# Kernel optimization log

Hardware: AMD Instinct MI355X
Metric: run time of the kernel (lower is better)

## Reference

```python
import jax, jax.numpy as jnp
import numpy as np
from jax import lax

LAGS = np.array([1, 2, 3, 4, 5, 6, 7, 14, 21, 28])
MAX_LAG = int(LAGS.max())
N_LAGS = len(LAGS)
HID = 512
EMB_ROWS, EMB_DIM = 12, 5
BATCH, CTX, HOR = 128, 720, 168
T0 = CTX + HOR + MAX_LAG  # 916
IN_DIM = 1 + N_LAGS + 1 + EMB_DIM  # target + lags + log-scale + seq-cat embedding = 17


def _lstm_cell(x, h, c, Wih, Whh, bih, bhh):
    g = x @ Wih.T + h @ Whh.T + bih + bhh
    i, f, gg, o = jnp.split(g, 4, axis=-1)  # torch gate order i,f,g,o
    c = jax.nn.sigmoid(f) * c + jax.nn.sigmoid(i) * jnp.tanh(gg)
    h = jax.nn.sigmoid(o) * jnp.tanh(c)
    return h, c


def _run_layer(xs, params):
    Bn = xs.shape[0]
    z = jnp.zeros((Bn, HID), xs.dtype)
    def step(hc, x):
        h, c = _lstm_cell(x, hc[0], hc[1], *params)
        return (h, c), h
    hc, ys = lax.scan(step, (z, z), jnp.swapaxes(xs, 0, 1))
    return jnp.swapaxes(ys, 0, 1), hc


def _forward(X, pad_mask, emb, W_ih0, W_hh0, b_ih0, b_hh0,
             W_ih1, W_hh1, b_ih1, b_hh1, W_head, b_head, H, C):
    Bn = X.shape[0]
    p0 = (W_ih0, W_hh0, b_ih0, b_hh0)
    p1 = (W_ih1, W_hh1, b_ih1, b_hh1)
    X = X.at[:, -H:, 0].set(0.0)
    past = X[:, :X.shape[1] - H, 0][:, ::-1]  # [B, C+MAX_LAG], newest first
    Xt = X[:, MAX_LAG:]                       # [B, T, 2], T = C + H
    mask = pad_mask[:, MAX_LAG:][:, :C].astype(X.dtype)
    scale = (jnp.abs(Xt[:, :C, 0]) * mask).sum(1) / jnp.clip(mask.sum(1), 1.0)
    scale = jnp.maximum(scale, 1e-10)         # [B]
    tgt = Xt[:, :, 0] / scale[:, None]        # scaled target
    past = past / scale[:, None]
    # context lag features: value at context step t is past[C-1-t]; lag l -> past[C-1-t+l]
    idx = (C - 1 - np.arange(C))[:, None] + LAGS[None, :]  # [C, N_LAGS], static
    lags_ctx = past[:, idx]                                # [B, C, N_LAGS]
    logscale = jnp.log(scale)[:, None]                     # [B, 1]
    seq_emb = emb[Xt[:, :, 1].astype(jnp.int32)]           # [B, T, EMB_DIM]
    x_ctx = jnp.concatenate([
        tgt[:, :C, None], lags_ctx,
        jnp.broadcast_to(logscale[:, None, :], (Bn, C, 1)),
        seq_emb[:, :C]], 2)                                # [B, C, IN_DIM]
    o1, hc1 = _run_layer(x_ctx, p0)
    o2, hc2 = _run_layer(o1, p1)
    y_ctx = o2 @ W_head.T + b_head                         # [B, C, 1]
    # per-step static decode features (log-scale + seq-cat embedding)
    feat_dec = jnp.concatenate([
        jnp.broadcast_to(logscale[:, None, :], (Bn, H - 1, 1)),
        seq_emb[:, C:C + H - 1]], 2)                       # [B, H-1, 1+EMB_DIM]
    lag_idx = LAGS - 1
    def dec_step(carry, feat):
        h1, c1, h2, c2, buf, prev = carry
        lag_t = buf[:, lag_idx]                            # [B, N_LAGS]
        # step input is clone().detach()'d in the original -> stop_gradient
        x_t = lax.stop_gradient(jnp.concatenate([prev[:, None], lag_t, feat], 1))
        h1, c1 = _lstm_cell(x_t, h1, c1, *p0)
        h2, c2 = _lstm_cell(h1, h2, c2, *p1)
        o = h2 @ W_head.T + b_head                         # [B, 1]
        buf = jnp.concatenate([prev[:, None], buf[:, :-1]], 1)
        return (h1, c1, h2, c2, buf, o[:, 0]), o
    carry0 = (hc1[0], hc1[1], hc2[0], hc2[1], past[:, :MAX_LAG], y_ctx[:, -1, 0])
    _, y_dec = lax.scan(dec_step, carry0, jnp.swapaxes(feat_dec, 0, 1))
    y_hat = jnp.concatenate([y_ctx, jnp.swapaxes(y_dec, 0, 1)], 1)  # [B, C+H-1, 1]
    return y_hat * scale[:, None, None]


def setup_inputs():
    key = jax.random.key(0)
    ks = jax.random.split(key, 10)
    s = 0.05
    tgt = jax.random.normal(ks[0], (BATCH, T0, 1), jnp.float32)
    cat = jax.random.randint(ks[1], (BATCH, T0, 1), 0, EMB_ROWS).astype(jnp.float32)
    return {
        "X": jnp.concatenate([tgt, cat], 2),
        "pad_mask": jnp.ones((BATCH, T0), dtype=bool),
        "emb": jax.random.normal(ks[2], (EMB_ROWS, EMB_DIM), jnp.float32) * s,
        "W_ih0": jax.random.normal(ks[3], (4 * HID, IN_DIM), jnp.float32) * s,
        "W_hh0": jax.random.normal(ks[4], (4 * HID, HID), jnp.float32) * s,
        "b_ih0": jnp.zeros((4 * HID,), jnp.float32),
        "b_hh0": jnp.zeros((4 * HID,), jnp.float32),
        "W_ih1": jax.random.normal(ks[5], (4 * HID, HID), jnp.float32) * s,
        "W_hh1": jax.random.normal(ks[6], (4 * HID, HID), jnp.float32) * s,
        "b_ih1": jnp.zeros((4 * HID,), jnp.float32),
        "b_hh1": jnp.zeros((4 * HID,), jnp.float32),
        "W_head": jax.random.normal(ks[7], (1, HID), jnp.float32) * s,
        "b_head": jnp.zeros((1,), jnp.float32),
        "H": HOR,
        "context_length": CTX,
    }


def reference(X, pad_mask, emb, W_ih0, W_hh0, b_ih0, b_hh0,
              W_ih1, W_hh1, b_ih1, b_hh1, W_head, b_head, H, context_length):
    return _forward(X, pad_mask, emb, W_ih0, W_hh0, b_ih0, b_hh0,
                    W_ih1, W_hh1, b_ih1, b_hh1, W_head, b_head, H, context_length)
```

## Files before the change

kernel.cpp:

```cpp
#include <hip/hip_runtime.h>
#include <math.h>


#define CTXL   720
#define MAXLAG 28
#define TT0    916
#define NSTEP  887
#define OUTW   887
#define HS2    (128 * 256)

typedef _Float16 h2v   __attribute__((ext_vector_type(2)));
typedef _Float16 half8 __attribute__((ext_vector_type(8)));
typedef float    f32x4 __attribute__((ext_vector_type(4)));

struct Prm {
  const float* __restrict__ Wih0; const float* __restrict__ Whh0;
  const float* __restrict__ bih0; const float* __restrict__ bhh0;
  const float* __restrict__ Wih1; const float* __restrict__ Whh1;
  const float* __restrict__ bih1; const float* __restrict__ bhh1;
  const float* __restrict__ Whead; const float* __restrict__ bhead;
  const float* __restrict__ scale; const float* __restrict__ ls;
  const float* __restrict__ V; const float* __restrict__ embf;
  unsigned* __restrict__ H0; unsigned* __restrict__ H1;
  float* __restrict__ Ypart;
  float* __restrict__ out;
  int* __restrict__ bar;
};

__device__ __forceinline__ void stb(float* p, float v) {
  __hip_atomic_store(p, v, __ATOMIC_RELAXED, __HIP_MEMORY_SCOPE_AGENT);
}
__device__ __forceinline__ void stbu(unsigned* p, unsigned v) {
  __hip_atomic_store(p, v, __ATOMIC_RELAXED, __HIP_MEMORY_SCOPE_AGENT);
}
__device__ __forceinline__ float ldb(const float* p) {
  return __hip_atomic_load(p, __ATOMIC_RELAXED, __HIP_MEMORY_SCOPE_AGENT);
}
__device__ __forceinline__ int ldbi(const int* p) {
  return __hip_atomic_load(p, __ATOMIC_RELAXED, __HIP_MEMORY_SCOPE_AGENT);
}
__device__ __forceinline__ uint2 ldbu2(const unsigned* p) {
  union { unsigned long long u; uint2 v; } cv;
  cv.u = __hip_atomic_load((const unsigned long long*)p, __ATOMIC_RELAXED,
                           __HIP_MEMORY_SCOPE_AGENT);
  return cv.v;
}
__device__ __forceinline__ float sigm(float x) {
  return __builtin_amdgcn_rcpf(1.f + __expf(-x));
}
__device__ __forceinline__ float tanh_f(float x) {
  return fmaf(2.f, __builtin_amdgcn_rcpf(1.f + __expf(-2.f * x)), -1.f);
}
__device__ __forceinline__ unsigned packh2(float a, float b) {
  union { h2v h; unsigned u; } cv;
  cv.h = h2v{(_Float16)a, (_Float16)b};
  return cv.u;
}

__global__ void prep_kernel(const float* __restrict__ X, const float* __restrict__ emb,
                            float* __restrict__ scale, float* __restrict__ ls,
                            float* __restrict__ V, float* __restrict__ embf,
                            unsigned* __restrict__ zb , int* __restrict__ bar)
{
    const int bid = blockIdx.x, tid = threadIdx.x;
    if (bid < 128) {
        const int b = bid;
        __shared__ float sred[256];
        __shared__ float s_scale;
        float p = 0.f;
        for (int t = tid; t < CTXL; t += 256)
            p += fabsf(X[(size_t)(b * TT0 + MAXLAG + t) * 2]);
        sred[tid] = p; __syncthreads();
        for (int s = 128; s > 0; s >>= 1) {
            if (tid < s) sred[tid] += sred[tid + s];
            __syncthreads();
        }
        if (tid == 0) {
            float sc = fmaxf(sred[0] / (float)CTXL, 1e-10f);
            s_scale = sc; scale[b] = sc; ls[b] = logf(sc);
        }
        __syncthreads();
        const float sc = s_scale;
        for (int j = tid; j < TT0 - 168; j += 256)
            V[(size_t)j * 128 + b] = X[(size_t)(b * TT0 + j) * 2] / sc;
        for (int t = tid; t < NSTEP; t += 256) {
            int cc = (int)X[(size_t)(b * TT0 + MAXLAG + t) * 2 + 1];
            #pragma unroll
            for (int d = 0; d < 5; ++d)
                embf[((size_t)t * 5 + d) * 128 + b] = emb[cc * 5 + d];
        }
    } else {
        const int ZT = 4 * HS2;
        for (int idx = (bid - 128) * 256 + tid; idx < ZT; idx += 128 * 256)
            zb[idx] = 0u;
        if (bid == 128) { bar[tid] = 0; bar[256 + tid] = 0; }
    }
}

#define STAGE(LDSBUF, GSRC) { _Pragma("unroll")                               \
    for (int r_ = 0; r_ < 2; ++r_) {                                          \
      const int ch_ = tid + r_ * 512;                                         \
      const int sl_ = ch_ >> 6, c_ = ch_ & 63;                                \
      const unsigned* gp_ = (GSRC) + (size_t)(S0 + sl_) * 256 + c_ * 4;       \
      const uint2 a_ = ldbu2(gp_), b_ = ldbu2(gp_ + 2);                       \
      *(uint4*)&(LDSBUF)[sl_ * 256 + ((c_ * 4) ^ ((sl_ & 7) << 2))] =         \
          make_uint4(a_.x, a_.y, b_.x, b_.y); } }

#define MMPASS_L1(D) { _Pragma("unroll")                                      \
    for (int t_ = 0; t_ < 16; ++t_) {                                         \
      union { uint4 u; half8 h; } b0_, b1_;                                   \
      b0_.u = *(const uint4*)&h0lds[ar * 256 + ((t_ * 16 + akg * 4) ^ xsw)];  \
      b1_.u = *(const uint4*)&h1lds[ar * 256 + ((t_ * 16 + akg * 4) ^ xsw)];  \
      D = __builtin_amdgcn_mfma_f32_16x16x32_f16(awA[t_], b0_.h, D, 0, 0, 0); \
      D = __builtin_amdgcn_mfma_f32_16x16x32_f16(awB[t_], b1_.h, D, 0, 0, 0); } }

#define MMPASS_L0(D) { _Pragma("unroll")                                      \
    for (int t_ = 0; t_ < 16; ++t_) {                                         \
      union { uint4 u; half8 h; } b0_;                                        \
      b0_.u = *(const uint4*)&h0lds[ar * 256 + ((t_ * 16 + akg * 4) ^ xsw)];  \
      D = __builtin_amdgcn_mfma_f32_16x16x32_f16(awA[t_], b0_.h, D, 0, 0, 0); } }

#define XDOT(G, XF) { const int ub_ = (T * 4 + akg) * 68;                     \
    _Pragma("unroll")                                                         \
    for (int q_ = 0; q_ < 4; ++q_) { float xd_ = b4[q_];                      \
      _Pragma("unroll")                                                       \
      for (int j_ = 0; j_ < 17; ++j_)                                         \
          xd_ = fmaf(sX0[ub_ + q_ * 17 + j_], (XF)[j_], xd_);                 \
      (G)[q_] += xd_; } }

#define OUTWRITE(PAR, STEP) {                                                 \
    float v_ = ldb(&p.Ypart[(size_t)(PAR) * 4096 + (S0 + (tid >> 5)) * 32 + (tid & 31)]); \
    v_ += __shfl_xor(v_, 1, 64); v_ += __shfl_xor(v_, 2, 64);                 \
    v_ += __shfl_xor(v_, 4, 64); v_ += __shfl_xor(v_, 8, 64);                 \
    v_ += __shfl_xor(v_, 16, 64);                                             \
    if ((l & 31) == 0)                                                        \
        stb(&p.out[(size_t)(S0 + (tid >> 5)) * OUTW + (STEP)],                \
            (v_ + bh_all) * sc_my); }

__global__ __launch_bounds__(512, 1) void deepar_persist(Prm p)
{
    const int tid = threadIdx.x, blk = blockIdx.x;
    const int ublk = blk >> 3, grp = blk & 7;
    const int U0 = ublk * 16, S0 = grp * 16;
    const int l = tid & 63, wv = tid >> 6;
    const int ar = l & 15, akg = l >> 4;
    const bool isL0 = (wv < 4);
    const int T = isL0 ? wv : (wv - 4);
    const int u = U0 + T * 4 + akg;
    const int sg = S0 + ar;
    const int xsw = (ar & 7) << 2;

    __shared__ unsigned h0lds[16 * 256];
    __shared__ unsigned h1lds[16 * 256];
    __shared__ float sX0[16 * 68];
    __shared__ float sYring[168 * 16];
    __shared__ float sYp[4][16];

    half8 awA[16], awB[16];
    {
        const int grow = ((ar & 3) << 9) + U0 + T * 4 + (ar >> 2);
        const float* srcA = isL0 ? p.Whh0 : p.Wih1;
        #pragma unroll
        for (int t = 0; t < 16; ++t) {
            #pragma unroll
            for (int j = 0; j < 8; ++j) {
                const int k = t * 32 + akg * 8 + j;
                awA[t][j] = (_Float16)srcA[(size_t)grow * 512 + k];
            }
        }
        if (!isL0) {
            #pragma unroll
            for (int t = 0; t < 16; ++t) {
                #pragma unroll
                for (int j = 0; j < 8; ++j) {
                    const int k = t * 32 + akg * 8 + j;
                    awB[t][j] = (_Float16)p.Whh1[(size_t)grow * 512 + k];
                }
            }
        }
    }
    for (int idx = tid; idx < 1088; idx += 512) {
        const int ul = idx / 68, r = idx % 68;
        const int q = r / 17, j = r % 17;
        sX0[idx] = p.Wih0[((q << 9) + U0 + ul) * 17 + j];
    }

    float cc = 0.f;
    float b4[4];
    float lsv = 0.f, whm = 0.f;
    if (isL0) {
        #pragma unroll
        for (int q = 0; q < 4; ++q)
            b4[q] = p.bih0[(q << 9) + u] + p.bhh0[(q << 9) + u];
        lsv = p.ls[sg];
    } else {
        #pragma unroll
        for (int q = 0; q < 4; ++q)
            b4[q] = p.bih1[(q << 9) + u] + p.bhh1[(q << 9) + u];
        whm = p.Whead[u];
    }
    const float bh_all = p.bhead[0];
    const float sc_my = p.scale[S0 + (tid >> 5)];
    __syncthreads();

    f32x4 g0c = {0.f, 0.f, 0.f, 0.f};
    int ph = 0;
    const int LG[10] = {1, 2, 3, 4, 5, 6, 7, 14, 21, 28};
    int* gctr = p.bar + grp * 64;

    auto gbar_arrive = [&]() {
        asm volatile("s_waitcnt vmcnt(0)" ::: "memory");
        __syncthreads();
        ++ph;
        if (wv == 7 && l == 0)
            __hip_atomic_fetch_add(&gctr[(ublk & 3) * 16], 1,
                                   __ATOMIC_RELAXED, __HIP_MEMORY_SCOPE_AGENT);
    };
    auto gbar_wait = [&]() {
        if (wv == 7) {
            const int target = 32 * ph;
            for (;;) {
                int v = (l < 4) ? ldbi(&gctr[l * 16]) : 0;
                v += __shfl_xor(v, 1, 64); v += __shfl_xor(v, 2, 64);
                if (__shfl(v, 0, 64) >= target) break;
                __builtin_amdgcn_s_sleep(1);
            }
        }
        __syncthreads();
    };

    for (int P = 0; P <= CTXL; ++P) {
        STAGE(h0lds, p.H0 + (size_t)((P - 1) & 1) * HS2);
        STAGE(h1lds, p.H1 + (size_t)(P & 1) * HS2);

        float xf[17];
        if (isL0 && P < CTXL) {
            xf[0] = p.V[(size_t)(MAXLAG + P) * 128 + sg];
            #pragma unroll
            for (int j = 0; j < 10; ++j)
                xf[1 + j] = p.V[(size_t)(MAXLAG + P - LG[j]) * 128 + sg];
            xf[11] = lsv;
            #pragma unroll
            for (int dd = 0; dd < 5; ++dd)
                xf[12 + dd] = p.embf[((size_t)P * 5 + dd) * 128 + sg];
        }
        __syncthreads();

        f32x4 d = {0.f, 0.f, 0.f, 0.f};
        if (isL0) { MMPASS_L0(d); } else { MMPASS_L1(d); }

        if (isL0) {
            if (P < CTXL) {
                float g[4] = { d[0], d[1], d[2], d[3] };
                XDOT(g, xf);
                const float ig = sigm(g[0]), fg = sigm(g[1]);
                const float gt = tanh_f(g[2]), og = sigm(g[3]);
                cc = fg * cc + ig * gt;
                const float h = og * tanh_f(cc);
                const float other = __shfl_xor(h, 16, 64);
                if (!(akg & 1))
                    stbu(&p.H0[(size_t)(P & 1) * HS2 + (size_t)sg * 256
                               + ublk * 8 + T * 2 + (akg >> 1)],
                         packh2(h, other));
            } else {
                g0c = d;
            }
        } else if (P >= 1) {
            float g[4] = { d[0] + b4[0], d[1] + b4[1], d[2] + b4[2], d[3] + b4[3] };
            const float ig = sigm(g[0]), fg = sigm(g[1]);
            const float gt = tanh_f(g[2]), og = sigm(g[3]);
            cc = fg * cc + ig * gt;
            const float h = og * tanh_f(cc);
            const float other = __shfl_xor(h, 16, 64);
            if (!(akg & 1))
                stbu(&p.H1[(size_t)((P - 1) & 1) * HS2 + (size_t)sg * 256
                           + ublk * 8 + T * 2 + (akg >> 1)],
                     packh2(h, other));
            float yp = whm * h;
            yp += __shfl_xor(yp, 16, 64);
            yp += __shfl_xor(yp, 32, 64);
            if (akg == 0) sYp[T][ar] = yp;
        }
        __syncthreads();
        if (P >= 1 && tid < 16) {
            const float ys = (sYp[0][tid] + sYp[1][tid]) + (sYp[2][tid] + sYp[3][tid]);
            stb(&p.Ypart[(size_t)((P - 1) & 1) * 4096 + (S0 + tid) * 32 + ublk], ys);
        }
        gbar_arrive();
        if (P >= 2 && ublk == (P & 31)) OUTWRITE(P & 1, P - 2);
        gbar_wait();
    }

    for (int t = CTXL; t < NSTEP; ++t) {
        {
            STAGE(h1lds, p.H1 + (size_t)((t - 1) & 1) * HS2);

            const int par = (t - 1) & 1;
            float v = ldb(&p.Ypart[(size_t)par * 4096 + (S0 + (tid >> 5)) * 32 + (tid & 31)]);
            v += __shfl_xor(v, 1, 64); v += __shfl_xor(v, 2, 64);
            v += __shfl_xor(v, 4, 64); v += __shfl_xor(v, 8, 64);
            v += __shfl_xor(v, 16, 64);
            if ((l & 31) == 0) {
                const float yv = v + bh_all;
                sYring[(t - CTXL) * 16 + (tid >> 5)] = yv;
                if (ublk == (t & 31))
                    stb(&p.out[(size_t)(S0 + (tid >> 5)) * OUTW + (t - 1)], yv * sc_my);
            }
            __syncthreads();

            if (isL0) {
                const float yprev = sYring[(t - CTXL) * 16 + ar];
                float xf[17];
                xf[0] = yprev;
                #pragma unroll
                for (int j = 0; j < 10; ++j) {
                    const int uu = t - LG[j];
                    const int ri = (uu - CTXL) < 0 ? 0 : (uu - CTXL);
                    xf[1 + j] = (uu < CTXL) ? p.V[(size_t)(MAXLAG + uu) * 128 + sg]
                                            : sYring[ri * 16 + ar];
                }
                xf[11] = lsv;
                #pragma unroll
                for (int dd = 0; dd < 5; ++dd)
                    xf[12 + dd] = p.embf[((size_t)t * 5 + dd) * 128 + sg];
                float g[4] = { g0c[0], g0c[1], g0c[2], g0c[3] };
                XDOT(g, xf);
                const float ig = sigm(g[0]), fg = sigm(g[1]);
                const float gt = tanh_f(g[2]), og = sigm(g[3]);
                cc = fg * cc + ig * gt;
                const float h = og * tanh_f(cc);
                const float other = __shfl_xor(h, 16, 64);
                if (!(akg & 1))
                    stbu(&p.H0[(size_t)(t & 1) * HS2 + (size_t)sg * 256
                               + ublk * 8 + T * 2 + (akg >> 1)],
                         packh2(h, other));
            }
            gbar_arrive();
            gbar_wait();
        }
        {
            STAGE(h0lds, p.H0 + (size_t)(t & 1) * HS2);
            __syncthreads();

            f32x4 d = {0.f, 0.f, 0.f, 0.f};
            if (isL0) { MMPASS_L0(d); } else { MMPASS_L1(d); }

            if (isL0) {
                g0c = d;
            } else {
                float g[4] = { d[0] + b4[0], d[1] + b4[1], d[2] + b4[2], d[3] + b4[3] };
                const float ig = sigm(g[0]), fg = sigm(g[1]);
                const float gt = tanh_f(g[2]), og = sigm(g[3]);
                cc = fg * cc + ig * gt;
                const float h = og * tanh_f(cc);
                const float other = __shfl_xor(h, 16, 64);
                if (!(akg & 1))
                    stbu(&p.H1[(size_t)(t & 1) * HS2 + (size_t)sg * 256
                               + ublk * 8 + T * 2 + (akg >> 1)],
                         packh2(h, other));
                float yp = whm * h;
                yp += __shfl_xor(yp, 16, 64);
                yp += __shfl_xor(yp, 32, 64);
                if (akg == 0) sYp[T][ar] = yp;
            }
            __syncthreads();
            if (tid < 16) {
                const float ys = (sYp[0][tid] + sYp[1][tid]) + (sYp[2][tid] + sYp[3][tid]);
                stb(&p.Ypart[(size_t)(t & 1) * 4096 + (S0 + tid) * 32 + ublk], ys);
            }
            gbar_arrive();
            gbar_wait();
        }
    }

    if (ublk == ((NSTEP - 1) & 31)) OUTWRITE(0, NSTEP - 1);
}

extern "C" void kernel_launch(void* const* d_in, const int* in_sizes, int n_in,
                              void* d_out, int out_size, void* d_ws, size_t ws_size,
                              hipStream_t stream)
{
    (void)in_sizes; (void)n_in; (void)out_size; (void)ws_size;
    const float* X   = (const float*)d_in[0];
    const float* emb = (const float*)d_in[2];
    Prm prm;
    prm.Wih0 = (const float*)d_in[3];
    prm.Whh0 = (const float*)d_in[4];
    prm.bih0 = (const float*)d_in[5];
    prm.bhh0 = (const float*)d_in[6];
    prm.Wih1 = (const float*)d_in[7];
    prm.Whh1 = (const float*)d_in[8];
    prm.bih1 = (const float*)d_in[9];
    prm.bhh1 = (const float*)d_in[10];
    prm.Whead = (const float*)d_in[11];
    prm.bhead = (const float*)d_in[12];
    float* out = (float*)d_out;

    float* ws    = (float*)d_ws;
    float* scale = ws;
    float* ls    = scale + 128;
    float* V     = ls + 128;
    float* embf  = V + 748 * 128;
    unsigned* H0 = (unsigned*)(embf + (size_t)888 * 5 * 128);
    unsigned* H1 = H0 + 2 * HS2;
    float* Ypart = (float*)(H1 + 2 * HS2);
    int*   bar   = (int*)(Ypart + 2 * 128 * 32);

    hipLaunchKernelGGL(prep_kernel, dim3(256), dim3(256), 0, stream,
                       X, emb, scale, ls, V, embf, H0, bar);

    prm.scale = scale; prm.ls = ls; prm.V = V; prm.embf = embf;
    prm.H0 = H0; prm.H1 = H1; prm.Ypart = Ypart; prm.out = out;
    prm.bar = bar;

    void* args[] = { &prm };
    hipLaunchCooperativeKernel((void*)deepar_persist, dim3(256), dim3(512),
                               args, 0, stream);
}
```

Baseline: 6.152 ms.

## Compute head output locally from staged h1 instead of cross-block partial sums

Removes the per-step Ypart global partial-sum exchange and its extra __syncthreads. Each block now recomputes the head projection directly from the full staged layer-1 hidden state in LDS, using fp16 dot2 against a packed copy of W_head. This drops one global write/read round-trip and one block barrier per step. In exchange every block does the full 512-wide dot product, the head now runs in fp16 inputs, and the context-phase output needs the staged h1, which may not be fully staged at that point.

```diff
diff --git a/kernel.cpp b/kernel.cpp
--- a/kernel.cpp
+++ b/kernel.cpp
@@ -22,7 +22,6 @@
   const float* __restrict__ scale; const float* __restrict__ ls;
   const float* __restrict__ V; const float* __restrict__ embf;
   unsigned* __restrict__ H0; unsigned* __restrict__ H1;
-  float* __restrict__ Ypart;
   float* __restrict__ out;
   int* __restrict__ bar;
 };
@@ -32,9 +31,6 @@
 }
 __device__ __forceinline__ void stbu(unsigned* p, unsigned v) {
   __hip_atomic_store(p, v, __ATOMIC_RELAXED, __HIP_MEMORY_SCOPE_AGENT);
-}
-__device__ __forceinline__ float ldb(const float* p) {
-  return __hip_atomic_load(p, __ATOMIC_RELAXED, __HIP_MEMORY_SCOPE_AGENT);
 }
 __device__ __forceinline__ int ldbi(const int* p) {
   return __hip_atomic_load(p, __ATOMIC_RELAXED, __HIP_MEMORY_SCOPE_AGENT);
@@ -55,6 +51,9 @@
   union { h2v h; unsigned u; } cv;
   cv.h = h2v{(_Float16)a, (_Float16)b};
   return cv.u;
+}
+__device__ __forceinline__ h2v ash2(unsigned u) {
+  union { unsigned u; h2v h; } cv; cv.u = u; return cv.h;
 }
 
 __global__ void prep_kernel(const float* __restrict__ X, const float* __restrict__ emb,
@@ -128,14 +127,20 @@
           xd_ = fmaf(sX0[ub_ + q_ * 17 + j_], (XF)[j_], xd_);                 \
       (G)[q_] += xd_; } }
 
-#define OUTWRITE(PAR, STEP) {                                                 \
-    float v_ = ldb(&p.Ypart[(size_t)(PAR) * 4096 + (S0 + (tid >> 5)) * 32 + (tid & 31)]); \
-    v_ += __shfl_xor(v_, 1, 64); v_ += __shfl_xor(v_, 2, 64);                 \
-    v_ += __shfl_xor(v_, 4, 64); v_ += __shfl_xor(v_, 8, 64);                 \
-    v_ += __shfl_xor(v_, 16, 64);                                             \
-    if ((l & 31) == 0)                                                        \
-        stb(&p.out[(size_t)(S0 + (tid >> 5)) * OUTW + (STEP)],                \
-            (v_ + bh_all) * sc_my); }
+#define YLOCAL(YV) {                                                          \
+    const int sl_ = tid >> 5, seg_ = tid & 31;                                \
+    const int msk_ = (sl_ & 7) << 2;                                          \
+    float a_ = 0.f;                                                           \
+    _Pragma("unroll")                                                         \
+    for (int j_ = 0; j_ < 8; ++j_) {                                          \
+      const int q_ = seg_ * 8 + j_;                                           \
+      a_ = __builtin_amdgcn_fdot2(ash2(h1lds[sl_ * 256 + (q_ ^ msk_)]),       \
+                                  ash2(sWh2[q_]), a_, false);                 \
+    }                                                                         \
+    a_ += __shfl_xor(a_, 1, 64);  a_ += __shfl_xor(a_, 2, 64);                \
+    a_ += __shfl_xor(a_, 4, 64);  a_ += __shfl_xor(a_, 8, 64);                \
+    a_ += __shfl_xor(a_, 16, 64);                                             \
+    YV = a_; }
 
 __global__ __launch_bounds__(512, 1) void deepar_persist(Prm p)
 {
@@ -152,9 +157,9 @@
 
     __shared__ unsigned h0lds[16 * 256];
     __shared__ unsigned h1lds[16 * 256];
+    __shared__ unsigned sWh2[256];
     __shared__ float sX0[16 * 68];
     __shared__ float sYring[168 * 16];
-    __shared__ float sYp[4][16];
 
     half8 awA[16], awB[16];
     {
@@ -184,10 +189,14 @@
         const int q = r / 17, j = r % 17;
         sX0[idx] = p.Wih0[((q << 9) + U0 + ul) * 17 + j];
     }
+    if (tid < 256) {
+        const int g = (tid >> 3) * 16 + ((tid & 7) >> 1) * 4 + (tid & 1) * 2;
+        sWh2[tid] = packh2(p.Whead[g], p.Whead[g + 1]);
+    }
 
     float cc = 0.f;
     float b4[4];
-    float lsv = 0.f, whm = 0.f;
+    float lsv = 0.f;
     if (isL0) {
         #pragma unroll
         for (int q = 0; q < 4; ++q)
@@ -197,7 +206,6 @@
         #pragma unroll
         for (int q = 0; q < 4; ++q)
             b4[q] = p.bih1[(q << 9) + u] + p.bhh1[(q << 9) + u];
-        whm = p.Whead[u];
     }
     const float bh_all = p.bhead[0];
     const float sc_my = p.scale[S0 + (tid >> 5)];
@@ -276,35 +284,29 @@
                 stbu(&p.H1[(size_t)((P - 1) & 1) * HS2 + (size_t)sg * 256
                            + ublk * 8 + T * 2 + (akg >> 1)],
                      packh2(h, other));
-            float yp = whm * h;
-            yp += __shfl_xor(yp, 16, 64);
-            yp += __shfl_xor(yp, 32, 64);
-            if (akg == 0) sYp[T][ar] = yp;
-        }
-        __syncthreads();
-        if (P >= 1 && tid < 16) {
-            const float ys = (sYp[0][tid] + sYp[1][tid]) + (sYp[2][tid] + sYp[3][tid]);
-            stb(&p.Ypart[(size_t)((P - 1) & 1) * 4096 + (S0 + tid) * 32 + ublk], ys);
         }
         gbar_arrive();
-        if (P >= 2 && ublk == (P & 31)) OUTWRITE(P & 1, P - 2);
+        if (P >= 2 && ublk == (P & 31)) {
+            float yv; YLOCAL(yv);
+            if ((tid & 31) == 0)
+                stb(&p.out[(size_t)(S0 + (tid >> 5)) * OUTW + (P - 2)],
+                    (yv + bh_all) * sc_my);
+        }
         gbar_wait();
     }
 
     for (int t = CTXL; t < NSTEP; ++t) {
         {
             STAGE(h1lds, p.H1 + (size_t)((t - 1) & 1) * HS2);
-
-            const int par = (t - 1) & 1;
-            float v = ldb(&p.Ypart[(size_t)par * 4096 + (S0 + (tid >> 5)) * 32 + (tid & 31)]);
-            v += __shfl_xor(v, 1, 64); v += __shfl_xor(v, 2, 64);
-            v += __shfl_xor(v, 4, 64); v += __shfl_xor(v, 8, 64);
-            v += __shfl_xor(v, 16, 64);
-            if ((l & 31) == 0) {
-                const float yv = v + bh_all;
-                sYring[(t - CTXL) * 16 + (tid >> 5)] = yv;
+            __syncthreads();
+
+            float yv; YLOCAL(yv);
+            if ((tid & 31) == 0) {
+                const float yw = yv + bh_all;
+                sYring[(t - CTXL) * 16 + (tid >> 5)] = yw;
                 if (ublk == (t & 31))
-                    stb(&p.out[(size_t)(S0 + (tid >> 5)) * OUTW + (t - 1)], yv * sc_my);
+                    stb(&p.out[(size_t)(S0 + (tid >> 5)) * OUTW + (t - 1)],
+                        yw * sc_my);
             }
             __syncthreads();
 
@@ -358,22 +360,20 @@
                     stbu(&p.H1[(size_t)(t & 1) * HS2 + (size_t)sg * 256
                                + ublk * 8 + T * 2 + (akg >> 1)],
                          packh2(h, other));
-                float yp = whm * h;
-                yp += __shfl_xor(yp, 16, 64);
-                yp += __shfl_xor(yp, 32, 64);
-                if (akg == 0) sYp[T][ar] = yp;
-            }
-            __syncthreads();
-            if (tid < 16) {
-                const float ys = (sYp[0][tid] + sYp[1][tid]) + (sYp[2][tid] + sYp[3][tid]);
-                stb(&p.Ypart[(size_t)(t & 1) * 4096 + (S0 + tid) * 32 + ublk], ys);
             }
             gbar_arrive();
             gbar_wait();
         }
     }
 
-    if (ublk == ((NSTEP - 1) & 31)) OUTWRITE(0, NSTEP - 1);
+    if (ublk == ((NSTEP - 1) & 31)) {
+        STAGE(h1lds, p.H1 + (size_t)0 * HS2);
+        __syncthreads();
+        float yv; YLOCAL(yv);
+        if ((tid & 31) == 0)
+            stb(&p.out[(size_t)(S0 + (tid >> 5)) * OUTW + (NSTEP - 1)],
+                (yv + bh_all) * sc_my);
+    }
 }
 
 extern "C" void kernel_launch(void* const* d_in, const int* in_sizes, int n_in,
@@ -403,14 +403,13 @@
     float* embf  = V + 748 * 128;
     unsigned* H0 = (unsigned*)(embf + (size_t)888 * 5 * 128);
     unsigned* H1 = H0 + 2 * HS2;
-    float* Ypart = (float*)(H1 + 2 * HS2);
-    int*   bar   = (int*)(Ypart + 2 * 128 * 32);
+    int*   bar   = (int*)(H1 + 2 * HS2);
 
     hipLaunchKernelGGL(prep_kernel, dim3(256), dim3(256), 0, stream,
                        X, emb, scale, ls, V, embf, H0, bar);
 
     prm.scale = scale; prm.ls = ls; prm.V = V; prm.embf = embf;
-    prm.H0 = H0; prm.H1 = H1; prm.Ypart = Ypart; prm.out = out;
+    prm.H0 = H0; prm.H1 = H1; prm.out = out;
     prm.bar = bar;
 
     void* args[] = { &prm };
```

After: 5.573 ms. -9.4%, faster.
